# Optimization experiments

Hardware: AMD Instinct MI355X
Metric: run time of the kernel (lower is better)

## Reference

```python
import jax, jax.numpy as jnp
import numpy as np

DIST_LAMBDA = 1.0
COL_LAMBDA = 0.5
WEIGHT_TILDA = [(1.0, 0.0), (0.4, 0.0048828125), (0.1, 0.009765625)]
EPS = 1e-7


def setup_inputs() -> dict:
    key = jax.random.key(0)
    k1, k2, k3, k4, k5 = jax.random.split(key, 5)
    N, A, T = 512, 128, 64
    pred_ego_traj = jax.random.normal(k1, (N, T, 2), dtype=jnp.float32)
    target_ego_traj = jax.random.normal(k2, (N, T, 2), dtype=jnp.float32)
    # box sizes must be positive (w, h); shift rand away from 0
    pred_ego_box_size = jax.random.uniform(k3, (N, 2), dtype=jnp.float32) + 0.1
    multiagent_box_sizes = jax.random.uniform(k4, (N, A, 2), dtype=jnp.float32) + 0.1
    multiagents_trajs = jax.random.normal(k5, (N, A, T, 2), dtype=jnp.float32)
    return {
        "pred_ego_traj": pred_ego_traj,
        "target_ego_traj": target_ego_traj,
        "pred_ego_box_size": pred_ego_box_size,
        "multiagent_box_sizes": multiagent_box_sizes,
        "multiagents_trajs": multiagents_trajs,
    }


def _ciou(x1, y1, w1, h1, x2, y2, w2, h2):
    """Complete IoU for center-format (x, y, w, h) boxes; args broadcast."""
    b1x1, b1x2 = x1 - w1 * 0.5, x1 + w1 * 0.5
    b1y1, b1y2 = y1 - h1 * 0.5, y1 + h1 * 0.5
    b2x1, b2x2 = x2 - w2 * 0.5, x2 + w2 * 0.5
    b2y1, b2y2 = y2 - h2 * 0.5, y2 + h2 * 0.5
    inter_w = jnp.clip(jnp.minimum(b1x2, b2x2) - jnp.maximum(b1x1, b2x1), 0.0)
    inter_h = jnp.clip(jnp.minimum(b1y2, b2y2) - jnp.maximum(b1y1, b2y1), 0.0)
    inter = inter_w * inter_h
    union = w1 * h1 + w2 * h2 - inter + EPS
    iou = inter / union
    # smallest enclosing box diagonal
    cw = jnp.maximum(b1x2, b2x2) - jnp.minimum(b1x1, b2x1)
    ch = jnp.maximum(b1y2, b2y2) - jnp.minimum(b1y1, b2y1)
    c2 = cw * cw + ch * ch + EPS
    rho2 = (x2 - x1) ** 2 + (y2 - y1) ** 2
    v = (4.0 / (jnp.pi ** 2)) * (jnp.arctan(w2 / (h2 + EPS)) - jnp.arctan(w1 / (h1 + EPS))) ** 2
    alpha = v / (1.0 - iou + v + EPS)
    return iou - rho2 / c2 - alpha * v


def reference(pred_ego_traj, target_ego_traj, pred_ego_box_size,
              multiagent_box_sizes, multiagents_trajs):
    # ---- distance loss (masked L2 over valid timesteps) ----
    valid = jnp.all(target_ego_traj != -999.0, axis=-1)  # (N, T) bool
    dist = jnp.sqrt(jnp.sum((pred_ego_traj - target_ego_traj) ** 2, axis=-1))  # (N, T)
    valid_f = valid.astype(dist.dtype)
    dist_loss = jnp.sum(dist * valid_f) / jnp.sum(valid_f)

    # ---- collision loss via broadcast (no materialized tiles) ----
    wt = jnp.asarray(WEIGHT_TILDA, dtype=multiagent_box_sizes.dtype)  # (K, 2)
    weights = wt[:, 0]   # (K,)
    tildas = wt[:, 1]    # (K,)
    # ego: (N, 1, 1, T)
    ex = pred_ego_traj[:, None, None, :, 0]
    ey = pred_ego_traj[:, None, None, :, 1]
    ew = pred_ego_box_size[:, None, None, None, 0]
    eh = pred_ego_box_size[:, None, None, None, 1]
    # agents: traj (N, A, 1, T), sizes padded per tilda -> (N, A, K, 1)
    ax = multiagents_trajs[:, :, None, :, 0]
    ay = multiagents_trajs[:, :, None, :, 1]
    aw = multiagent_box_sizes[:, :, None, None, 0] + tildas[None, None, :, None]
    ah = multiagent_box_sizes[:, :, None, None, 1] + tildas[None, None, :, None]

    ciou = _ciou(ex, ey, ew, eh, ax, ay, aw, ah)  # (N, A, K, T)
    mask = valid[:, None, None, :]                 # (N, 1, 1, T)
    ciou = jnp.where(mask, ciou, 0.0)
    denom = jnp.sum(mask.astype(ciou.dtype), axis=-1)  # (N, 1, 1)
    ciou_t = jnp.sum(ciou, axis=-1) / denom            # (N, A, K)
    col = jnp.sum(ciou_t * weights[None, None, :], axis=-1)  # (N, A)
    col_loss = jnp.mean(col)

    return DIST_LAMBDA * dist_loss + COL_LAMBDA * col_loss
```

## Files before the change

### kernel.cpp

```cpp
#include <hip/hip_runtime.h>
#include <math.h>

#define EPSF 1e-7f
#define NN 512
#define AA 128
#define TT 64

#define FOUR_OVER_PI2 0.40528473456935109f

__device__ __forceinline__ float fast_rcp(float x) {
    return __builtin_amdgcn_rcpf(x);
}

__global__ __launch_bounds__(256) void plan_loss_main(
    const float* __restrict__ pe,
    const float* __restrict__ te,
    const float* __restrict__ ebox,
    const float* __restrict__ abox,
    const float* __restrict__ atraj,
    float* __restrict__ ws_col,
    float* __restrict__ ws_dist,
    float* __restrict__ ws_valid)
{
    __shared__ float s_ex[TT], s_ey[TT];
    __shared__ float s_bx1[TT], s_bx2[TT], s_by1[TT], s_by2[TT];
    __shared__ float s_vf[TT];
    __shared__ float s_awh[64][3], s_ahh[64][3], s_area[64][3], s_v2[64][3], s_opv[64][3];
    __shared__ float s_wsum[4];
    __shared__ float s_den;

    const int bid = blockIdx.x;
    const int n   = bid >> 1;
    const int s   = bid & 1;
    const int tid = threadIdx.x;
    const int agentBase = s * 64;

    const float ew = ebox[n*2 + 0];
    const float eh = ebox[n*2 + 1];

    if (tid < 64) {
        const int t = tid;
        const float px = pe[(n*TT + t)*2 + 0];
        const float py = pe[(n*TT + t)*2 + 1];
        const float tx = te[(n*TT + t)*2 + 0];
        const float ty = te[(n*TT + t)*2 + 1];
        const float vf = (tx != -999.0f && ty != -999.0f) ? 1.0f : 0.0f;
        const float dx = px - tx, dy = py - ty;
        const float dist = sqrtf(dx*dx + dy*dy);
        const float hw = ew * 0.5f, hh = eh * 0.5f;
        s_ex[t] = px;       s_ey[t] = py;
        s_bx1[t] = px - hw; s_bx2[t] = px + hw;
        s_by1[t] = py - hh; s_by2[t] = py + hh;
        s_vf[t] = vf;
        float rd = dist * vf, rv = vf;
        #pragma unroll
        for (int o = 32; o >= 1; o >>= 1) {
            rd += __shfl_xor(rd, o);
            rv += __shfl_xor(rv, o);
        }
        if (t == 0) {
            s_den = rv;
            if (s == 0) { ws_dist[n] = rd; ws_valid[n] = rv; }
        }
    } else if (tid < 128) {
        const int la = tid - 64;
        const int a  = agentBase + la;
        const float bw = abox[(n*AA + a)*2 + 0];
        const float bh = abox[(n*AA + a)*2 + 1];
        const float area1 = ew * eh;
        const float atane = atanf(ew / (eh + EPSF));
        const float tld[3] = {0.0f, 0.0048828125f, 0.009765625f};
        #pragma unroll
        for (int w = 0; w < 3; w++) {
            const float aw = bw + tld[w];
            const float ah = bh + tld[w];
            s_awh[la][w]  = aw * 0.5f;
            s_ahh[la][w]  = ah * 0.5f;
            s_area[la][w] = area1 + aw*ah + EPSF;
            const float d = atanf(aw / (ah + EPSF)) - atane;
            const float v = FOUR_OVER_PI2 * d * d;
            s_v2[la][w]  = v * v;
            s_opv[la][w] = 1.0f + v + EPSF;
        }
    }
    __syncthreads();

    const int la = tid >> 2;
    const int q  = tid & 3;
    const int a  = agentBase + la;

    float awhR[3], ahhR[3], areaR[3], v2R[3], opvR[3];
    #pragma unroll
    for (int w = 0; w < 3; w++) {
        awhR[w]  = s_awh[la][w];
        ahhR[w]  = s_ahh[la][w];
        areaR[w] = s_area[la][w];
        v2R[w]   = s_v2[la][w];
        opvR[w]  = s_opv[la][w];
    }

    const float4* tp = reinterpret_cast<const float4*>(
        atraj + ((size_t)(n*AA + a)) * TT * 2) + q * 8;

    float acc0 = 0.0f, acc1 = 0.0f, acc2 = 0.0f;

    #pragma unroll
    for (int j = 0; j < 8; j++) {
        const float4 p = tp[j];
        const int t0 = (q*8 + j) * 2;

        #pragma unroll
        for (int half = 0; half < 2; half++) {
            const int t = t0 + half;
            const float ax = half ? p.z : p.x;
            const float ay = half ? p.w : p.y;

            const float bx1 = s_bx1[t], bx2 = s_bx2[t];
            const float by1 = s_by1[t], by2 = s_by2[t];
            const float exv = s_ex[t],  eyv = s_ey[t];
            const float vf  = s_vf[t];

            const float ddx = ax - exv, ddy = ay - eyv;
            const float rho2 = ddx*ddx + ddy*ddy;

            float res[3];
            #pragma unroll
            for (int w = 0; w < 3; w++) {
                const float b2x1 = ax - awhR[w], b2x2 = ax + awhR[w];
                const float b2y1 = ay - ahhR[w], b2y2 = ay + ahhR[w];
                float iw = fminf(bx2, b2x2) - fmaxf(bx1, b2x1);
                float ih = fminf(by2, b2y2) - fmaxf(by1, b2y1);
                iw = fmaxf(iw, 0.0f);
                ih = fmaxf(ih, 0.0f);
                const float inter = iw * ih;
                const float uni = areaR[w] - inter;
                const float iou = inter * fast_rcp(uni);
                const float cw = fmaxf(bx2, b2x2) - fminf(bx1, b2x1);
                const float ch = fmaxf(by2, b2y2) - fminf(by1, b2y1);
                const float c2 = cw*cw + ch*ch + EPSF;
                res[w] = iou - rho2 * fast_rcp(c2) - v2R[w] * fast_rcp(opvR[w] - iou);
            }
            acc0 += vf * res[0];
            acc1 += vf * res[1];
            acc2 += vf * res[2];
        }
    }

    float cacc = 1.0f*acc0 + 0.4f*acc1 + 0.1f*acc2;
    #pragma unroll
    for (int o = 32; o >= 1; o >>= 1) cacc += __shfl_xor(cacc, o);

    const int wave = tid >> 6;
    const int lane = tid & 63;
    if (lane == 0) s_wsum[wave] = cacc;
    __syncthreads();
    if (tid == 0) {
        const float tot = s_wsum[0] + s_wsum[1] + s_wsum[2] + s_wsum[3];
        ws_col[bid] = tot / s_den;
    }
}

__global__ __launch_bounds__(512) void plan_loss_final(
    const float* __restrict__ ws_col,
    const float* __restrict__ ws_dist,
    const float* __restrict__ ws_valid,
    float* __restrict__ out)
{
    __shared__ float sd[8], sv[8], sc[8];
    const int tid = threadIdx.x;
    float d = ws_dist[tid];
    float v = ws_valid[tid];
    float c = ws_col[tid] + ws_col[tid + 512];
    #pragma unroll
    for (int o = 32; o >= 1; o >>= 1) {
        d += __shfl_xor(d, o);
        v += __shfl_xor(v, o);
        c += __shfl_xor(c, o);
    }
    const int wave = tid >> 6, lane = tid & 63;
    if (lane == 0) { sd[wave] = d; sv[wave] = v; sc[wave] = c; }
    __syncthreads();
    if (tid == 0) {
        float Sd = 0.0f, Sv = 0.0f, Sc = 0.0f;
        #pragma unroll
        for (int i = 0; i < 8; i++) { Sd += sd[i]; Sv += sv[i]; Sc += sc[i]; }
        out[0] = 1.0f * (Sd / Sv) + 0.5f * (Sc * (1.0f / 65536.0f));
    }
}

extern "C" void kernel_launch(void* const* d_in, const int* in_sizes, int n_in,
                              void* d_out, int out_size, void* d_ws, size_t ws_size,
                              hipStream_t stream) {
    const float* pe    = (const float*)d_in[0];
    const float* te    = (const float*)d_in[1];
    const float* ebox  = (const float*)d_in[2];
    const float* abox  = (const float*)d_in[3];
    const float* atraj = (const float*)d_in[4];

    float* wsf      = (float*)d_ws;
    float* ws_col   = wsf;
    float* ws_dist  = wsf + 1024;
    float* ws_valid = wsf + 1536;

    plan_loss_main<<<NN*2, 256, 0, stream>>>(pe, te, ebox, abox, atraj,
                                             ws_col, ws_dist, ws_valid);
    plan_loss_final<<<1, 512, 0, stream>>>(ws_col, ws_dist, ws_valid, (float*)d_out);
}
```

Before: 94.30 us.

## Fuse final reduction into main kernel via last-block flag spin-wait

```diff
diff --git a/kernel.cpp b/kernel.cpp
--- a/kernel.cpp
+++ b/kernel.cpp
@@ -5,22 +5,26 @@
 #define NN 512
 #define AA 128
 #define TT 64
+#define NBLK (NN*2)
 
 #define FOUR_OVER_PI2 0.40528473456935109f
+#define FLAG_MAGIC 0x1CEB00DAu
 
 __device__ __forceinline__ float fast_rcp(float x) {
     return __builtin_amdgcn_rcpf(x);
 }
 
-__global__ __launch_bounds__(256) void plan_loss_main(
+__global__ __launch_bounds__(256, 4) void plan_loss_fused(
     const float* __restrict__ pe,
     const float* __restrict__ te,
     const float* __restrict__ ebox,
     const float* __restrict__ abox,
     const float* __restrict__ atraj,
-    float* __restrict__ ws_col,
+    float* __restrict__ ws_part,
     float* __restrict__ ws_dist,
-    float* __restrict__ ws_valid)
+    float* __restrict__ ws_valid,
+    unsigned int* __restrict__ flags,
+    float* __restrict__ out)
 {
     __shared__ float s_ex[TT], s_ey[TT];
     __shared__ float s_bx1[TT], s_bx2[TT], s_by1[TT], s_by2[TT];
@@ -28,12 +32,22 @@
     __shared__ float s_awh[64][3], s_ahh[64][3], s_area[64][3], s_v2[64][3], s_opv[64][3];
     __shared__ float s_wsum[4];
     __shared__ float s_den;
+    __shared__ float s_fin[3][4];
 
     const int bid = blockIdx.x;
     const int n   = bid >> 1;
     const int s   = bid & 1;
     const int tid = threadIdx.x;
     const int agentBase = s * 64;
+
+    const int la = tid >> 2;
+    const int q  = tid & 3;
+    const int a  = agentBase + la;
+    const float4* tp = reinterpret_cast<const float4*>(
+        atraj + ((size_t)(n*AA + a)) * TT * 2) + q * 8;
+    float4 p[8];
+    #pragma unroll
+    for (int j = 0; j < 8; j++) p[j] = tp[j];
 
     const float ew = ebox[n*2 + 0];
     const float eh = ebox[n*2 + 1];
@@ -60,13 +74,16 @@
         }
         if (t == 0) {
             s_den = rv;
-            if (s == 0) { ws_dist[n] = rd; ws_valid[n] = rv; }
+            if (s == 0) {
+                __hip_atomic_store(&ws_dist[n],  rd, __ATOMIC_RELAXED, __HIP_MEMORY_SCOPE_AGENT);
+                __hip_atomic_store(&ws_valid[n], rv, __ATOMIC_RELAXED, __HIP_MEMORY_SCOPE_AGENT);
+            }
         }
     } else if (tid < 128) {
-        const int la = tid - 64;
-        const int a  = agentBase + la;
-        const float bw = abox[(n*AA + a)*2 + 0];
-        const float bh = abox[(n*AA + a)*2 + 1];
+        const int lla = tid - 64;
+        const int aa  = agentBase + lla;
+        const float bw = abox[(n*AA + aa)*2 + 0];
+        const float bh = abox[(n*AA + aa)*2 + 1];
         const float area1 = ew * eh;
         const float atane = atanf(ew / (eh + EPSF));
         const float tld[3] = {0.0f, 0.0048828125f, 0.009765625f};
@@ -74,20 +91,16 @@
         for (int w = 0; w < 3; w++) {
             const float aw = bw + tld[w];
             const float ah = bh + tld[w];
-            s_awh[la][w]  = aw * 0.5f;
-            s_ahh[la][w]  = ah * 0.5f;
-            s_area[la][w] = area1 + aw*ah + EPSF;
+            s_awh[lla][w]  = aw * 0.5f;
+            s_ahh[lla][w]  = ah * 0.5f;
+            s_area[lla][w] = area1 + aw*ah + EPSF;
             const float d = atanf(aw / (ah + EPSF)) - atane;
             const float v = FOUR_OVER_PI2 * d * d;
-            s_v2[la][w]  = v * v;
-            s_opv[la][w] = 1.0f + v + EPSF;
+            s_v2[lla][w]  = v * v;
+            s_opv[lla][w] = 1.0f + v + EPSF;
         }
     }
     __syncthreads();
-
-    const int la = tid >> 2;
-    const int q  = tid & 3;
-    const int a  = agentBase + la;
 
     float awhR[3], ahhR[3], areaR[3], v2R[3], opvR[3];
     #pragma unroll
@@ -99,21 +112,16 @@
         opvR[w]  = s_opv[la][w];
     }
 
-    const float4* tp = reinterpret_cast<const float4*>(
-        atraj + ((size_t)(n*AA + a)) * TT * 2) + q * 8;
-
     float acc0 = 0.0f, acc1 = 0.0f, acc2 = 0.0f;
 
     #pragma unroll
     for (int j = 0; j < 8; j++) {
-        const float4 p = tp[j];
         const int t0 = (q*8 + j) * 2;
-
         #pragma unroll
         for (int half = 0; half < 2; half++) {
             const int t = t0 + half;
-            const float ax = half ? p.z : p.x;
-            const float ay = half ? p.w : p.y;
+            const float ax = half ? p[j].z : p[j].x;
+            const float ay = half ? p[j].w : p[j].y;
 
             const float bx1 = s_bx1[t], bx2 = s_bx2[t];
             const float by1 = s_by1[t], by2 = s_by2[t];
@@ -146,7 +154,7 @@
         }
     }
 
-    float cacc = 1.0f*acc0 + 0.4f*acc1 + 0.1f*acc2;
+    float cacc = acc0 + 0.4f*acc1 + 0.1f*acc2;
     #pragma unroll
     for (int o = 32; o >= 1; o >>= 1) cacc += __shfl_xor(cacc, o);
 
@@ -156,35 +164,50 @@
     __syncthreads();
     if (tid == 0) {
         const float tot = s_wsum[0] + s_wsum[1] + s_wsum[2] + s_wsum[3];
-        ws_col[bid] = tot / s_den;
-    }
-}
-
-__global__ __launch_bounds__(512) void plan_loss_final(
-    const float* __restrict__ ws_col,
-    const float* __restrict__ ws_dist,
-    const float* __restrict__ ws_valid,
-    float* __restrict__ out)
-{
-    __shared__ float sd[8], sv[8], sc[8];
-    const int tid = threadIdx.x;
-    float d = ws_dist[tid];
-    float v = ws_valid[tid];
-    float c = ws_col[tid] + ws_col[tid + 512];
-    #pragma unroll
-    for (int o = 32; o >= 1; o >>= 1) {
-        d += __shfl_xor(d, o);
-        v += __shfl_xor(v, o);
-        c += __shfl_xor(c, o);
-    }
-    const int wave = tid >> 6, lane = tid & 63;
-    if (lane == 0) { sd[wave] = d; sv[wave] = v; sc[wave] = c; }
-    __syncthreads();
-    if (tid == 0) {
-        float Sd = 0.0f, Sv = 0.0f, Sc = 0.0f;
-        #pragma unroll
-        for (int i = 0; i < 8; i++) { Sd += sd[i]; Sv += sv[i]; Sc += sc[i]; }
-        out[0] = 1.0f * (Sd / Sv) + 0.5f * (Sc * (1.0f / 65536.0f));
+        __hip_atomic_store(&ws_part[bid], tot * fast_rcp(s_den),
+                           __ATOMIC_RELAXED, __HIP_MEMORY_SCOPE_AGENT);
+        __hip_atomic_store(&flags[bid], FLAG_MAGIC ^ (unsigned)bid,
+                           __ATOMIC_RELEASE, __HIP_MEMORY_SCOPE_AGENT);
+    }
+
+    if (bid == NBLK - 1) {
+        const int f0 = tid * 4;
+        #pragma unroll
+        for (int k = 0; k < 4; k++) {
+            const unsigned f = (unsigned)(f0 + k);
+            const unsigned expv = FLAG_MAGIC ^ f;
+            while (__hip_atomic_load(&flags[f], __ATOMIC_ACQUIRE,
+                                     __HIP_MEMORY_SCOPE_AGENT) != expv) {
+                __builtin_amdgcn_s_sleep(2);
+            }
+        }
+        __syncthreads();
+
+        float c = 0.0f, d = 0.0f, v = 0.0f;
+        #pragma unroll
+        for (int k = 0; k < 4; k++)
+            c += __hip_atomic_load(&ws_part[f0 + k], __ATOMIC_RELAXED, __HIP_MEMORY_SCOPE_AGENT);
+        #pragma unroll
+        for (int k = 0; k < 2; k++) {
+            d += __hip_atomic_load(&ws_dist[tid*2 + k],  __ATOMIC_RELAXED, __HIP_MEMORY_SCOPE_AGENT);
+            v += __hip_atomic_load(&ws_valid[tid*2 + k], __ATOMIC_RELAXED, __HIP_MEMORY_SCOPE_AGENT);
+        }
+        #pragma unroll
+        for (int o = 32; o >= 1; o >>= 1) {
+            c += __shfl_xor(c, o);
+            d += __shfl_xor(d, o);
+            v += __shfl_xor(v, o);
+        }
+        if (lane == 0) { s_fin[0][wave] = c; s_fin[1][wave] = d; s_fin[2][wave] = v; }
+        __syncthreads();
+        if (tid == 0) {
+            float Sc = 0.0f, Sd = 0.0f, Sv = 0.0f;
+            #pragma unroll
+            for (int i = 0; i < 4; i++) {
+                Sc += s_fin[0][i]; Sd += s_fin[1][i]; Sv += s_fin[2][i];
+            }
+            out[0] = Sd / Sv + 0.5f * (Sc * (1.0f / 65536.0f));
+        }
     }
 }
 
@@ -197,12 +220,13 @@
     const float* abox  = (const float*)d_in[3];
     const float* atraj = (const float*)d_in[4];
 
-    float* wsf      = (float*)d_ws;
-    float* ws_col   = wsf;
-    float* ws_dist  = wsf + 1024;
-    float* ws_valid = wsf + 1536;
-
-    plan_loss_main<<<NN*2, 256, 0, stream>>>(pe, te, ebox, abox, atraj,
-                                             ws_col, ws_dist, ws_valid);
-    plan_loss_final<<<1, 512, 0, stream>>>(ws_col, ws_dist, ws_valid, (float*)d_out);
+    float* wsf            = (float*)d_ws;
+    float* ws_part        = wsf;
+    float* ws_dist        = wsf + 1024;
+    float* ws_valid       = wsf + 1536;
+    unsigned int* flags   = (unsigned int*)(wsf + 2048);
+
+    plan_loss_fused<<<NBLK, 256, 0, stream>>>(pe, te, ebox, abox, atraj,
+                                              ws_part, ws_dist, ws_valid,
+                                              flags, (float*)d_out);
 }
```

Measured after the change: 97.08 us. +2.9%, slower.
